# Performance work log

Measured on AMD Instinct MI355X. Metric: run time of the kernel, lower is better.

Reference implementation:

```python
import jax, jax.numpy as jnp
import numpy as np

C, G = 128, 2000          # num_cells, total_genes
CE, GE, H = 64, 64, 256   # cell_embed_dim, gene_embed_dim, hidden_dim
F = CE + GE + 3           # FCGNN input: ctrl val + cell_embed + gene_embed + shift + num_cells


def setup_inputs() -> dict:
    key = jax.random.key(0)
    ks = jax.random.split(key, 13)
    s = 0.02
    return {
        "ctrl": jax.random.uniform(ks[0], (C, G), dtype=jnp.float32),
        "shift_vec": jax.random.normal(ks[1], (G,), dtype=jnp.float32),
        "gene_indices": jnp.arange(G, dtype=jnp.int32),
        # CellEmbedding params
        "ce_w1": jax.random.normal(ks[2], (G, H), dtype=jnp.float32) * s,
        "ce_b1": jnp.zeros((H,), dtype=jnp.float32),
        "ce_w2": jax.random.normal(ks[3], (H, CE), dtype=jnp.float32) * s,
        "ce_b2": jnp.zeros((CE,), dtype=jnp.float32),
        # gene embedding table
        "gene_table": jax.random.normal(ks[4], (G, GE), dtype=jnp.float32) * s,
        # FCGNN params
        "g_w1": jax.random.normal(ks[5], (F, H), dtype=jnp.float32) * s,
        "g_b1": jnp.zeros((H,), dtype=jnp.float32),
        "g_w2": jax.random.normal(ks[6], (2 * H, H), dtype=jnp.float32) * s,
        "g_b2": jnp.zeros((H,), dtype=jnp.float32),
        "g_w3": jax.random.normal(ks[7], (2 * H, 1), dtype=jnp.float32) * s,
        "g_b3": jnp.zeros((1,), dtype=jnp.float32),
    }


def reference(ctrl, shift_vec, gene_indices, ce_w1, ce_b1, ce_w2, ce_b2,
              gene_table, g_w1, g_b1, g_w2, g_b2, g_w3, g_b3):
    num_cells = ctrl.shape[0]
    num_genes = gene_indices.shape[0]

    # CellEmbedding: fc2(elu(fc1(ctrl)))  -> [C, CE]
    ce = jax.nn.elu(ctrl @ ce_w1 + ce_b1) @ ce_w2 + ce_b2

    ctrl_g = ctrl[:, gene_indices]           # [C, Gn]
    shift = shift_vec[gene_indices]          # [Gn]
    ge = gene_table[gene_indices]            # [Gn, GE]

    # Build [C, Gn, F] feature tensor (ctrl val, cell embed, gene embed, shift, num_cells)
    z = jnp.concatenate([
        ctrl_g[:, :, None],
        jnp.broadcast_to(ce[:, None, :], (num_cells, num_genes, ce.shape[1])),
        jnp.broadcast_to(ge[None, :, :], (num_cells, num_genes, ge.shape[1])),
        jnp.broadcast_to(shift[None, :, None], (num_cells, num_genes, 1)),
        jnp.full((num_cells, num_genes, 1), float(num_cells), dtype=ctrl.dtype),
    ], axis=2)

    # FCGNN applied per gene (vectorized over gene axis); pooling is mean over cells (axis 0)
    x = jax.nn.elu(z @ g_w1 + g_b1)                                   # [C, Gn, H]
    p = x.mean(axis=0)                                                # [Gn, H]
    x = jnp.concatenate([x, jnp.broadcast_to(p[None], x.shape)], -1) @ g_w2 + g_b2
    p = x.mean(axis=0)
    x = jax.nn.elu(jnp.concatenate([x, jnp.broadcast_to(p[None], x.shape)], -1)) @ g_w3 + g_b3
    out = x[..., 0]                                                   # [C, Gn]

    # softmax over cells (torch Softmax(dim=0) after transpose/squeeze)
    return jax.nn.softmax(out, axis=0)
```

## Files before the change

### kernel.cpp

```cpp
#include <hip/hip_runtime.h>
#include <math.h>

#define G_GENES 2000
#define C_CELLS 128
#define H_DIM   256
#define CE_DIM  64
#define LDAe    260

typedef __attribute__((ext_vector_type(8))) short short8;
typedef __attribute__((ext_vector_type(4))) float floatx4;

__device__ __forceinline__ float eluf(float x) {
    float e = __expf(x) - 1.0f;
    return x > 0.0f ? x : e;
}
__device__ __forceinline__ unsigned short f2bf(float v) {
    unsigned u = __float_as_uint(v);
    u += 0x7FFF + ((u >> 16) & 1);
    return (unsigned short)(u >> 16);
}

__global__ __launch_bounds__(1024) void k_prep(
    const float* __restrict__ ctrl, const float* __restrict__ ce_w1,
    const float* __restrict__ ce_b1, const float* __restrict__ ce_w2,
    const float* __restrict__ ce_b2, const float* __restrict__ g_w1,
    const float* __restrict__ g_b1, const float* __restrict__ shiftv,
    const int* __restrict__ gidx, const float* __restrict__ gtab,
    const float* __restrict__ g_w2,
    float* __restrict__ Atc, unsigned short* __restrict__ w2abt,
    float* __restrict__ Bvg)
{
    const int b = blockIdx.x;
    const int t = threadIdx.x;

    if (b < 64) {
        __shared__ float crow[2][G_GENES];
        __shared__ float hidp[4][2][H_DIM];
        __shared__ float hid[2][H_DIM];
        __shared__ float celp[16][2][CE_DIM];
        __shared__ float cel[2][CE_DIM];
        const int c0 = b * 2;
        for (int i = t; i < G_GENES; i += 1024) {
            crow[0][i] = ctrl[(size_t)c0 * G_GENES + i];
            crow[1][i] = ctrl[(size_t)(c0 + 1) * G_GENES + i];
        }
        __syncthreads();

        {
            const int h = t & 255, kq = t >> 8;
            float a0 = 0.f, a1 = 0.f, b0 = 0.f, b1 = 0.f;
            const float* w = ce_w1 + (size_t)(kq * 500) * H_DIM + h;
            const float* r0 = crow[0] + kq * 500;
            const float* r1 = crow[1] + kq * 500;
            #pragma unroll 5
            for (int k = 0; k < 500; k += 2) {
                float w0 = w[(size_t)k * H_DIM];
                float w1v = w[(size_t)(k + 1) * H_DIM];
                a0 = fmaf(r0[k], w0, a0);     b0 = fmaf(r1[k], w0, b0);
                a1 = fmaf(r0[k + 1], w1v, a1); b1 = fmaf(r1[k + 1], w1v, b1);
            }
            hidp[kq][0][h] = a0 + a1;
            hidp[kq][1][h] = b0 + b1;
        }
        __syncthreads();
        if (t < 512) {
            const int cc_ = t >> 8, h = t & 255;
            hid[cc_][h] = eluf(hidp[0][cc_][h] + hidp[1][cc_][h] + hidp[2][cc_][h]
                             + hidp[3][cc_][h] + ce_b1[h]);
        }
        __syncthreads();

        {
            const int e = t & 63, grp = t >> 6;
            float c0p = 0.f, c1p = 0.f;
            #pragma unroll
            for (int hh = 0; hh < 16; ++hh) {
                const int h = grp * 16 + hh;
                float wv = ce_w2[(size_t)h * CE_DIM + e];
                c0p = fmaf(hid[0][h], wv, c0p);
                c1p = fmaf(hid[1][h], wv, c1p);
            }
            celp[grp][0][e] = c0p;
            celp[grp][1][e] = c1p;
        }
        __syncthreads();
        if (t < 128) {
            const int cc_ = t >> 6, e = t & 63;
            float s = ce_b2[e];
            #pragma unroll
            for (int grp = 0; grp < 16; ++grp) s += celp[grp][cc_][e];
            cel[cc_][e] = s;
        }
        __syncthreads();
        if (t < 512) {
            const int cc_ = t >> 8, h = t & 255;
            float a = 0.f;
            #pragma unroll 8
            for (int e = 0; e < CE_DIM; ++e)
                a = fmaf(cel[cc_][e], g_w1[(size_t)(1 + e) * H_DIM + h], a);
            Atc[(size_t)(c0 + cc_) * H_DIM + h] = a;
        }
    } else if (b < 72) {
        const int n  = (b - 64) * 32 + (t >> 5);
        const int k0 = (t & 31) * 8;
        unsigned v[8];
        #pragma unroll
        for (int j = 0; j < 8; ++j) v[j] = f2bf(g_w2[(size_t)(k0 + j) * H_DIM + n]);
        uint4 pk;
        pk.x = v[0] | (v[1] << 16);
        pk.y = v[2] | (v[3] << 16);
        pk.z = v[4] | (v[5] << 16);
        pk.w = v[6] | (v[7] << 16);
        *(uint4*)&w2abt[(size_t)n * H_DIM + k0] = pk;
    } else {
        const int g = (b - 72) * 4 + (t >> 8);
        const int h = t & 255;
        const int idx = gidx[g];
        float bv = g_b1[h] + 128.0f * g_w1[(size_t)130 * H_DIM + h]
                 + shiftv[idx] * g_w1[(size_t)129 * H_DIM + h];
        #pragma unroll 8
        for (int e = 0; e < CE_DIM; ++e)
            bv = fmaf(gtab[(size_t)idx * CE_DIM + e], g_w1[(size_t)(65 + e) * H_DIM + h], bv);
        Bvg[(size_t)g * H_DIM + h] = bv;
    }
}

__global__ __launch_bounds__(1024) void k_pq(
    const float* __restrict__ ctrl, const int* __restrict__ gidx,
    const float* __restrict__ g_w1, const float* __restrict__ g_w2,
    const float* __restrict__ g_b2, const float* __restrict__ Atc,
    const float* __restrict__ Bvg, float* __restrict__ q_all)
{
    __shared__ float ccl[C_CELLS][8];
    __shared__ float pp[4][8][H_DIM];
    __shared__ float pf[8][H_DIM];

    const int g0 = blockIdx.x * 8;
    const int t = threadIdx.x;

    {
        const int c = t >> 3, gg = t & 7;
        if (t < 1024) ccl[c][gg] = ctrl[(size_t)c * G_GENES + gidx[g0 + gg]];
    }
    __syncthreads();

    const int h = t & 255, cq = t >> 8;
    {
        const float w1h = g_w1[h];
        float bv[8];
        #pragma unroll
        for (int gg = 0; gg < 8; ++gg) bv[gg] = Bvg[(size_t)(g0 + gg) * H_DIM + h];
        float s[8];
        #pragma unroll
        for (int gg = 0; gg < 8; ++gg) s[gg] = 0.f;
        for (int ci = 0; ci < 32; ++ci) {
            const int c = cq * 32 + ci;
            const float at = Atc[(size_t)c * H_DIM + h];
            #pragma unroll
            for (int gg = 0; gg < 8; ++gg)
                s[gg] += eluf(fmaf(ccl[c][gg], w1h, at + bv[gg]));
        }
        #pragma unroll
        for (int gg = 0; gg < 8; ++gg) pp[cq][gg][h] = s[gg];
    }
    __syncthreads();

    {
        const int i = t, gg = i >> 7, hh2 = (i & 127) * 2;
        #pragma unroll
        for (int u = 0; u < 2; ++u) {
            const int hh = hh2 + u;
            pf[gg][hh] = (pp[0][gg][hh] + pp[1][gg][hh] + pp[2][gg][hh] + pp[3][gg][hh])
                         * (1.0f / 128.0f);
        }
    }
    __syncthreads();

    {
        const int j = t & 255, gp = t >> 8;
        float q0 = g_b2[j], q1 = g_b2[j];
        const float* w2b = g_w2 + (size_t)H_DIM * H_DIM + j;
        const float* p0 = pf[gp * 2];
        const float* p1 = pf[gp * 2 + 1];
        #pragma unroll 8
        for (int hh = 0; hh < H_DIM; ++hh) {
            const float wv = w2b[(size_t)hh * H_DIM];
            q0 = fmaf(p0[hh], wv, q0);
            q1 = fmaf(p1[hh], wv, q1);
        }
        q_all[(size_t)(g0 + gp * 2) * H_DIM + j] = q0;
        q_all[(size_t)(g0 + gp * 2 + 1) * H_DIM + j] = q1;
    }
}

__global__ __launch_bounds__(512, 4) void k_main(
    const float* __restrict__ ctrl, const int* __restrict__ gidx,
    const float* __restrict__ g_w1, const float* __restrict__ g_w3,
    const float* __restrict__ Atc, const float* __restrict__ Bvg,
    const float* __restrict__ q_all, const unsigned short* __restrict__ w2abt,
    float* __restrict__ out)
{
    __shared__ __align__(16) unsigned short x1t[C_CELLS * LDAe];
    __shared__ float red2[C_CELLS * 5];
    __shared__ __align__(16) float Bvl[H_DIM];
    __shared__ __align__(16) float w1l[H_DIM];
    __shared__ float qv[H_DIM];
    __shared__ float w3v[H_DIM];
    __shared__ float cc[C_CELLS];
    __shared__ float wred[4];

    const int g = blockIdx.x;
    const int t = threadIdx.x;
    const int idx = gidx[g];

    const int lane = t & 63;
    const int w    = t >> 6;
    const int quad = lane >> 4;
    const int nlo  = lane & 15;
    const int wm   = w >> 2;
    const int wn   = w & 3;

    const unsigned short* bbase = w2abt + (size_t)(wn * 64 + nlo) * H_DIM + quad * 8;
    short8 bcur[4];
    #pragma unroll
    for (int nt = 0; nt < 4; ++nt)
        bcur[nt] = *(const short8*)(bbase + (size_t)nt * 16 * H_DIM);

    if (t < C_CELLS) cc[t] = ctrl[(size_t)t * G_GENES + idx];
    if (t < H_DIM) {
        Bvl[t] = Bvg[(size_t)g * H_DIM + t];
        w1l[t] = g_w1[t];
        qv[t]  = q_all[(size_t)g * H_DIM + t];
        w3v[t] = g_w3[t];
    }
    __syncthreads();

    {
        const int ho = t & 31, cgrp = t >> 5;
        const int h0 = ho * 8;
        float4 wv0 = *(const float4*)(w1l + h0);
        float4 wv1 = *(const float4*)(w1l + h0 + 4);
        float4 bv0 = *(const float4*)(Bvl + h0);
        float4 bv1 = *(const float4*)(Bvl + h0 + 4);
        #pragma unroll
        for (int i = 0; i < 8; ++i) {
            const int c = cgrp * 8 + i;
            const float ccv = cc[c];
            float4 a0 = *(const float4*)(Atc + (size_t)c * H_DIM + h0);
            float4 a1 = *(const float4*)(Atc + (size_t)c * H_DIM + h0 + 4);
            float v0 = eluf(fmaf(ccv, wv0.x, a0.x + bv0.x));
            float v1 = eluf(fmaf(ccv, wv0.y, a0.y + bv0.y));
            float v2 = eluf(fmaf(ccv, wv0.z, a0.z + bv0.z));
            float v3 = eluf(fmaf(ccv, wv0.w, a0.w + bv0.w));
            float v4 = eluf(fmaf(ccv, wv1.x, a1.x + bv1.x));
            float v5 = eluf(fmaf(ccv, wv1.y, a1.y + bv1.y));
            float v6 = eluf(fmaf(ccv, wv1.z, a1.z + bv1.z));
            float v7 = eluf(fmaf(ccv, wv1.w, a1.w + bv1.w));
            uint4 pk;
            pk.x = (unsigned)f2bf(v0) | ((unsigned)f2bf(v1) << 16);
            pk.y = (unsigned)f2bf(v2) | ((unsigned)f2bf(v3) << 16);
            pk.z = (unsigned)f2bf(v4) | ((unsigned)f2bf(v5) << 16);
            pk.w = (unsigned)f2bf(v6) | ((unsigned)f2bf(v7) << 16);
            *(uint4*)&x1t[c * LDAe + h0] = pk;
        }
    }
    __syncthreads();

    floatx4 acc[4][4];
    #pragma unroll
    for (int mt = 0; mt < 4; ++mt)
        #pragma unroll
        for (int nt = 0; nt < 4; ++nt)
            acc[mt][nt] = (floatx4){0.f, 0.f, 0.f, 0.f};

    const unsigned short* abase = &x1t[(wm * 64 + nlo) * LDAe + quad * 8];

    #pragma unroll
    for (int kt = 0; kt < 8; ++kt) {
        short8 af[4];
        #pragma unroll
        for (int mt = 0; mt < 4; ++mt)
            af[mt] = *(const short8*)(abase + mt * 16 * LDAe + kt * 32);
        short8 bnx[4];
        if (kt < 7) {
            #pragma unroll
            for (int nt = 0; nt < 4; ++nt)
                bnx[nt] = *(const short8*)(bbase + (size_t)nt * 16 * H_DIM + (kt + 1) * 32);
        }
        #pragma unroll
        for (int nt = 0; nt < 4; ++nt)
            #pragma unroll
            for (int mt = 0; mt < 4; ++mt)
                acc[mt][nt] = __builtin_amdgcn_mfma_f32_16x16x32_bf16(af[mt], bcur[nt], acc[mt][nt], 0, 0, 0);
        if (kt < 7) {
            #pragma unroll
            for (int nt = 0; nt < 4; ++nt) bcur[nt] = bnx[nt];
        }
    }

    float qj[4], w3j[4];
    #pragma unroll
    for (int nt = 0; nt < 4; ++nt) {
        const int j = wn * 64 + nt * 16 + nlo;
        qj[nt] = qv[j];
        w3j[nt] = w3v[j];
    }
    #pragma unroll
    for (int mt = 0; mt < 4; ++mt) {
        #pragma unroll
        for (int reg = 0; reg < 4; ++reg) {
            float part = 0.f;
            #pragma unroll
            for (int nt = 0; nt < 4; ++nt)
                part = fmaf(eluf(acc[mt][nt][reg] + qj[nt]), w3j[nt], part);
            part += __shfl_xor(part, 1);
            part += __shfl_xor(part, 2);
            part += __shfl_xor(part, 4);
            part += __shfl_xor(part, 8);
            if (nlo == 0)
                red2[(wm * 64 + mt * 16 + quad * 4 + reg) * 5 + wn] = part;
        }
    }
    __syncthreads();

    float s = 0.f, e = 0.f;
    if (t < C_CELLS) {
        s = red2[t * 5 + 0] + red2[t * 5 + 1] + red2[t * 5 + 2] + red2[t * 5 + 3];
        float m = s;
        #pragma unroll
        for (int off = 1; off < 64; off <<= 1) m = fmaxf(m, __shfl_xor(m, off));
        if (lane == 0) wred[w] = m;
    }
    __syncthreads();
    if (t < C_CELLS) {
        const float m = fmaxf(wred[0], wred[1]);
        e = __expf(s - m);
        float S = e;
        #pragma unroll
        for (int off = 1; off < 64; off <<= 1) S += __shfl_xor(S, off);
        if (lane == 0) wred[2 + w] = S;
    }
    __syncthreads();
    if (t < C_CELLS) out[(size_t)t * G_GENES + g] = e / (wred[2] + wred[3]);
}

extern "C" void kernel_launch(void* const* d_in, const int* in_sizes, int n_in,
                              void* d_out, int out_size, void* d_ws, size_t ws_size,
                              hipStream_t stream) {
    const float* ctrl   = (const float*)d_in[0];
    const float* shiftv = (const float*)d_in[1];
    const int*   gidx   = (const int*)d_in[2];
    const float* ce_w1  = (const float*)d_in[3];
    const float* ce_b1  = (const float*)d_in[4];
    const float* ce_w2  = (const float*)d_in[5];
    const float* ce_b2  = (const float*)d_in[6];
    const float* gtab   = (const float*)d_in[7];
    const float* g_w1   = (const float*)d_in[8];
    const float* g_b1   = (const float*)d_in[9];
    const float* g_w2   = (const float*)d_in[10];
    const float* g_b2   = (const float*)d_in[11];
    const float* g_w3   = (const float*)d_in[12];

    char* ws = (char*)d_ws;
    float* Atc            = (float*)(ws);
    unsigned short* w2abt = (unsigned short*)(ws + 128 * 1024);
    float* Bvg            = (float*)(ws + 256 * 1024);
    float* q_all          = (float*)(ws + 256 * 1024 + (size_t)G_GENES * H_DIM * 4);
    float* out            = (float*)d_out;

    k_prep<<<64 + 8 + G_GENES / 4, 1024, 0, stream>>>(
        ctrl, ce_w1, ce_b1, ce_w2, ce_b2, g_w1, g_b1, shiftv, gidx, gtab, g_w2,
        Atc, w2abt, Bvg);
    k_pq<<<G_GENES / 8, 1024, 0, stream>>>(ctrl, gidx, g_w1, g_w2, g_b2, Atc, Bvg, q_all);
    k_main<<<G_GENES, 512, 0, stream>>>(ctrl, gidx, g_w1, g_w3, Atc, Bvg, q_all, w2abt, out);
}
```

Measured before the change: 238.7 us.

## Compute cell-embedding fc1 with bf16 MFMA split-K and separate finish kernel

Replaces the scalar FP32 ctrl@ce_w1 GEMV-style prep with a split-K bf16 MFMA GEMM over 16 K-chunks, writing partial sums to workspace. A new small kernel reduces the partials and finishes ELU, fc2 and the g_w1 projection per cell. Bf16 packing switches to the library conversion intrinsic. This adds a kernel launch and a partial-sum round-trip through memory, and lowers the precision of the cell-embedding matmul.

Result: faster. 232.6 us (-2.6%).

```diff
diff --git a/kernel.cpp b/kernel.cpp
--- a/kernel.cpp
+++ b/kernel.cpp
@@ -1,4 +1,5 @@
 #include <hip/hip_runtime.h>
+#include <hip/hip_bf16.h>
 #include <math.h>
 
 #define G_GENES 2000
@@ -6,6 +7,7 @@
 #define H_DIM   256
 #define CE_DIM  64
 #define LDAe    260
+#define LDBt    132
 
 typedef __attribute__((ext_vector_type(8))) short short8;
 typedef __attribute__((ext_vector_type(4))) float floatx4;
@@ -19,101 +21,105 @@
     u += 0x7FFF + ((u >> 16) & 1);
     return (unsigned short)(u >> 16);
 }
-
-__global__ __launch_bounds__(1024) void k_prep(
+__device__ __forceinline__ unsigned pk2(float a, float b) {
+    __hip_bfloat162 h2 = __float22bfloat162_rn(make_float2(a, b));
+    unsigned r; __builtin_memcpy(&r, &h2, 4); return r;
+}
+union U8 { unsigned u[4]; short8 s; uint4 v; };
+
+__global__ __launch_bounds__(512) void k_g1(
     const float* __restrict__ ctrl, const float* __restrict__ ce_w1,
-    const float* __restrict__ ce_b1, const float* __restrict__ ce_w2,
-    const float* __restrict__ ce_b2, const float* __restrict__ g_w1,
-    const float* __restrict__ g_b1, const float* __restrict__ shiftv,
-    const int* __restrict__ gidx, const float* __restrict__ gtab,
-    const float* __restrict__ g_w2,
-    float* __restrict__ Atc, unsigned short* __restrict__ w2abt,
+    const float* __restrict__ g_w1, const float* __restrict__ g_b1,
+    const float* __restrict__ shiftv, const int* __restrict__ gidx,
+    const float* __restrict__ gtab, const float* __restrict__ g_w2,
+    float* __restrict__ hidpart, unsigned short* __restrict__ w2abt,
     float* __restrict__ Bvg)
 {
     const int b = blockIdx.x;
     const int t = threadIdx.x;
 
-    if (b < 64) {
-        __shared__ float crow[2][G_GENES];
-        __shared__ float hidp[4][2][H_DIM];
-        __shared__ float hid[2][H_DIM];
-        __shared__ float celp[16][2][CE_DIM];
-        __shared__ float cel[2][CE_DIM];
-        const int c0 = b * 2;
-        for (int i = t; i < G_GENES; i += 1024) {
-            crow[0][i] = ctrl[(size_t)c0 * G_GENES + i];
-            crow[1][i] = ctrl[(size_t)(c0 + 1) * G_GENES + i];
+    if (b < 16) {
+        __shared__ __align__(16) unsigned short bt[H_DIM * LDBt];
+        const int kb = b * 128;
+        {
+            const int kk = t >> 2;
+            const int hq = t & 3;
+            const bool valid = (kb + kk) < G_GENES;
+            const float* src = ce_w1 + (size_t)(kb + kk) * H_DIM + hq * 64;
+            #pragma unroll
+            for (int j = 0; j < 64; j += 8) {
+                float4 f0 = {0.f,0.f,0.f,0.f}, f1 = {0.f,0.f,0.f,0.f};
+                if (valid) { f0 = *(const float4*)(src + j); f1 = *(const float4*)(src + j + 4); }
+                const int hb = hq * 64 + j;
+                bt[(hb + 0) * LDBt + kk] = f2bf(f0.x);
+                bt[(hb + 1) * LDBt + kk] = f2bf(f0.y);
+                bt[(hb + 2) * LDBt + kk] = f2bf(f0.z);
+                bt[(hb + 3) * LDBt + kk] = f2bf(f0.w);
+                bt[(hb + 4) * LDBt + kk] = f2bf(f1.x);
+                bt[(hb + 5) * LDBt + kk] = f2bf(f1.y);
+                bt[(hb + 6) * LDBt + kk] = f2bf(f1.z);
+                bt[(hb + 7) * LDBt + kk] = f2bf(f1.w);
+            }
         }
         __syncthreads();
 
-        {
-            const int h = t & 255, kq = t >> 8;
-            float a0 = 0.f, a1 = 0.f, b0 = 0.f, b1 = 0.f;
-            const float* w = ce_w1 + (size_t)(kq * 500) * H_DIM + h;
-            const float* r0 = crow[0] + kq * 500;
-            const float* r1 = crow[1] + kq * 500;
-            #pragma unroll 5
-            for (int k = 0; k < 500; k += 2) {
-                float w0 = w[(size_t)k * H_DIM];
-                float w1v = w[(size_t)(k + 1) * H_DIM];
-                a0 = fmaf(r0[k], w0, a0);     b0 = fmaf(r1[k], w0, b0);
-                a1 = fmaf(r0[k + 1], w1v, a1); b1 = fmaf(r1[k + 1], w1v, b1);
+        const int lane = t & 63, w = t >> 6;
+        const int quad = lane >> 4, nlo = lane & 15;
+        const int wm = w >> 2, wn = w & 3;
+
+        floatx4 acc[4][4];
+        #pragma unroll
+        for (int mt = 0; mt < 4; ++mt)
+            #pragma unroll
+            for (int nt = 0; nt < 4; ++nt) acc[mt][nt] = (floatx4){0.f,0.f,0.f,0.f};
+
+        #pragma unroll
+        for (int kt = 0; kt < 4; ++kt) {
+            const int kl = kt * 32 + quad * 8;
+            int kg = kb + kl; if (kg > G_GENES - 8) kg = 1992;
+            short8 af[4];
+            #pragma unroll
+            for (int mt = 0; mt < 4; ++mt) {
+                const int row = wm * 64 + mt * 16 + nlo;
+                const float* ap = ctrl + (size_t)row * G_GENES + kg;
+                float4 a0 = *(const float4*)ap;
+                float4 a1 = *(const float4*)(ap + 4);
+                U8 u;
+                u.u[0] = pk2(a0.x, a0.y); u.u[1] = pk2(a0.z, a0.w);
+                u.u[2] = pk2(a1.x, a1.y); u.u[3] = pk2(a1.z, a1.w);
+                af[mt] = u.s;
             }
-            hidp[kq][0][h] = a0 + a1;
-            hidp[kq][1][h] = b0 + b1;
-        }
-        __syncthreads();
-        if (t < 512) {
-            const int cc_ = t >> 8, h = t & 255;
-            hid[cc_][h] = eluf(hidp[0][cc_][h] + hidp[1][cc_][h] + hidp[2][cc_][h]
-                             + hidp[3][cc_][h] + ce_b1[h]);
-        }
-        __syncthreads();
-
-        {
-            const int e = t & 63, grp = t >> 6;
-            float c0p = 0.f, c1p = 0.f;
-            #pragma unroll
-            for (int hh = 0; hh < 16; ++hh) {
-                const int h = grp * 16 + hh;
-                float wv = ce_w2[(size_t)h * CE_DIM + e];
-                c0p = fmaf(hid[0][h], wv, c0p);
-                c1p = fmaf(hid[1][h], wv, c1p);
+            #pragma unroll
+            for (int nt = 0; nt < 4; ++nt) {
+                short8 bf = *(const short8*)&bt[(wn * 64 + nt * 16 + nlo) * LDBt + kl];
+                #pragma unroll
+                for (int mt = 0; mt < 4; ++mt)
+                    acc[mt][nt] = __builtin_amdgcn_mfma_f32_16x16x32_bf16(af[mt], bf, acc[mt][nt], 0, 0, 0);
             }
-            celp[grp][0][e] = c0p;
-            celp[grp][1][e] = c1p;
-        }
-        __syncthreads();
-        if (t < 128) {
-            const int cc_ = t >> 6, e = t & 63;
-            float s = ce_b2[e];
-            #pragma unroll
-            for (int grp = 0; grp < 16; ++grp) s += celp[grp][cc_][e];
-            cel[cc_][e] = s;
-        }
-        __syncthreads();
-        if (t < 512) {
-            const int cc_ = t >> 8, h = t & 255;
-            float a = 0.f;
-            #pragma unroll 8
-            for (int e = 0; e < CE_DIM; ++e)
-                a = fmaf(cel[cc_][e], g_w1[(size_t)(1 + e) * H_DIM + h], a);
-            Atc[(size_t)(c0 + cc_) * H_DIM + h] = a;
-        }
-    } else if (b < 72) {
-        const int n  = (b - 64) * 32 + (t >> 5);
+        }
+        #pragma unroll
+        for (int mt = 0; mt < 4; ++mt)
+            #pragma unroll
+            for (int nt = 0; nt < 4; ++nt) {
+                const int col = wn * 64 + nt * 16 + nlo;
+                #pragma unroll
+                for (int reg = 0; reg < 4; ++reg) {
+                    const int row = wm * 64 + mt * 16 + quad * 4 + reg;
+                    hidpart[((size_t)b * C_CELLS + row) * H_DIM + col] = acc[mt][nt][reg];
+                }
+            }
+    } else if (b < 32) {
+        const int n  = (b - 16) * 16 + (t >> 5);
         const int k0 = (t & 31) * 8;
-        unsigned v[8];
-        #pragma unroll
-        for (int j = 0; j < 8; ++j) v[j] = f2bf(g_w2[(size_t)(k0 + j) * H_DIM + n]);
-        uint4 pk;
-        pk.x = v[0] | (v[1] << 16);
-        pk.y = v[2] | (v[3] << 16);
-        pk.z = v[4] | (v[5] << 16);
-        pk.w = v[6] | (v[7] << 16);
-        *(uint4*)&w2abt[(size_t)n * H_DIM + k0] = pk;
+        float v[8];
+        #pragma unroll
+        for (int j = 0; j < 8; ++j) v[j] = g_w2[(size_t)(k0 + j) * H_DIM + n];
+        U8 u;
+        u.u[0] = pk2(v[0], v[1]); u.u[1] = pk2(v[2], v[3]);
+        u.u[2] = pk2(v[4], v[5]); u.u[3] = pk2(v[6], v[7]);
+        *(uint4*)&w2abt[(size_t)n * H_DIM + k0] = u.v;
     } else {
-        const int g = (b - 72) * 4 + (t >> 8);
+        const int g = (b - 32) * 2 + (t >> 8);
         const int h = t & 255;
         const int idx = gidx[g];
         float bv = g_b1[h] + 128.0f * g_w1[(size_t)130 * H_DIM + h]
@@ -123,6 +129,43 @@
             bv = fmaf(gtab[(size_t)idx * CE_DIM + e], g_w1[(size_t)(65 + e) * H_DIM + h], bv);
         Bvg[(size_t)g * H_DIM + h] = bv;
     }
+}
+
+__global__ __launch_bounds__(256) void k_fin(
+    const float* __restrict__ hidpart, const float* __restrict__ ce_b1,
+    const float* __restrict__ ce_w2, const float* __restrict__ ce_b2,
+    const float* __restrict__ g_w1, float* __restrict__ Atc)
+{
+    __shared__ float hid[H_DIM];
+    __shared__ float celp[4 * CE_DIM];
+    __shared__ float cel[CE_DIM];
+    const int c = blockIdx.x;
+    const int t = threadIdx.x;
+
+    float s = ce_b1[t];
+    #pragma unroll
+    for (int kc = 0; kc < 16; ++kc)
+        s += hidpart[((size_t)kc * C_CELLS + c) * H_DIM + t];
+    hid[t] = eluf(s);
+    __syncthreads();
+
+    {
+        const int e = t & 63, q4 = t >> 6;
+        float cp = 0.f;
+        #pragma unroll 8
+        for (int hh = 0; hh < 64; ++hh)
+            cp = fmaf(hid[q4 * 64 + hh], ce_w2[(size_t)(q4 * 64 + hh) * CE_DIM + e], cp);
+        celp[q4 * CE_DIM + e] = cp;
+    }
+    __syncthreads();
+    if (t < CE_DIM)
+        cel[t] = ce_b2[t] + celp[t] + celp[CE_DIM + t] + celp[2 * CE_DIM + t] + celp[3 * CE_DIM + t];
+    __syncthreads();
+
+    float a = 0.f;
+    #pragma unroll 8
+    for (int e = 0; e < CE_DIM; ++e) a = fmaf(cel[e], g_w1[(size_t)(1 + e) * H_DIM + t], a);
+    Atc[(size_t)c * H_DIM + t] = a;
 }
 
 __global__ __launch_bounds__(1024) void k_pq(
@@ -140,7 +183,7 @@
 
     {
         const int c = t >> 3, gg = t & 7;
-        if (t < 1024) ccl[c][gg] = ctrl[(size_t)c * G_GENES + gidx[g0 + gg]];
+        ccl[c][gg] = ctrl[(size_t)c * G_GENES + gidx[g0 + gg]];
     }
     __syncthreads();
 
@@ -166,7 +209,7 @@
     __syncthreads();
 
     {
-        const int i = t, gg = i >> 7, hh2 = (i & 127) * 2;
+        const int gg = t >> 7, hh2 = (t & 127) * 2;
         #pragma unroll
         for (int u = 0; u < 2; ++u) {
             const int hh = hh2 + u;
@@ -257,10 +300,8 @@
             float v6 = eluf(fmaf(ccv, wv1.z, a1.z + bv1.z));
             float v7 = eluf(fmaf(ccv, wv1.w, a1.w + bv1.w));
             uint4 pk;
-            pk.x = (unsigned)f2bf(v0) | ((unsigned)f2bf(v1) << 16);
-            pk.y = (unsigned)f2bf(v2) | ((unsigned)f2bf(v3) << 16);
-            pk.z = (unsigned)f2bf(v4) | ((unsigned)f2bf(v5) << 16);
-            pk.w = (unsigned)f2bf(v6) | ((unsigned)f2bf(v7) << 16);
+            pk.x = pk2(v0, v1); pk.y = pk2(v2, v3);
+            pk.z = pk2(v4, v5); pk.w = pk2(v6, v7);
             *(uint4*)&x1t[c * LDAe + h0] = pk;
         }
     }
@@ -366,11 +407,12 @@
     unsigned short* w2abt = (unsigned short*)(ws + 128 * 1024);
     float* Bvg            = (float*)(ws + 256 * 1024);
     float* q_all          = (float*)(ws + 256 * 1024 + (size_t)G_GENES * H_DIM * 4);
+    float* hidpart        = q_all;
     float* out            = (float*)d_out;
 
-    k_prep<<<64 + 8 + G_GENES / 4, 1024, 0, stream>>>(
-        ctrl, ce_w1, ce_b1, ce_w2, ce_b2, g_w1, g_b1, shiftv, gidx, gtab, g_w2,
-        Atc, w2abt, Bvg);
+    k_g1<<<32 + G_GENES / 2, 512, 0, stream>>>(
+        ctrl, ce_w1, g_w1, g_b1, shiftv, gidx, gtab, g_w2, hidpart, w2abt, Bvg);
+    k_fin<<<C_CELLS, 256, 0, stream>>>(hidpart, ce_b1, ce_w2, ce_b2, g_w1, Atc);
     k_pq<<<G_GENES / 8, 1024, 0, stream>>>(ctrl, gidx, g_w1, g_w2, g_b2, Atc, Bvg, q_all);
     k_main<<<G_GENES, 512, 0, stream>>>(ctrl, gidx, g_w1, g_w3, Atc, Bvg, q_all, w2abt, out);
 }
```
